# Kernel optimization log

Hardware: AMD Instinct MI355X
Metric: run time of the kernel (lower is better)

Reference implementation:

```python
import jax, jax.numpy as jnp
import numpy as np

NUM_HEADS = 16
EPS = 1e-6


def setup_inputs() -> dict:
    key = jax.random.key(0)
    ks = jax.random.split(key, 5)
    L, N, E = 2048, 8, 1024
    scale = 1.0 / np.sqrt(E)
    return {
        "query": jax.random.normal(ks[0], (L, N, E), jnp.float32),
        "Wq": jax.random.normal(ks[1], (E, E), jnp.float32) * scale,
        "Wk": jax.random.normal(ks[2], (E, E), jnp.float32) * scale,
        "Wv": jax.random.normal(ks[3], (E, E), jnp.float32) * scale,
        "Wo": jax.random.normal(ks[4], (E, E), jnp.float32) * scale,
    }


def reference(query, Wq, Wk, Wv, Wo):
    # cosFormer non-causal linear attention (self.causal = False branch).
    L, N, E = query.shape
    h = NUM_HEADS
    d = E // h

    # projections (nn.Linear, no bias) + ReLU feature map on q, k
    q = jax.nn.relu(query @ Wq.T)
    k = jax.nn.relu(query @ Wk.T)  # key defaults to query
    v = query @ Wv.T               # value defaults to query

    # (L, N, E) -> (n = N*h, L, d)
    def split_heads(x):
        return x.reshape(L, N * h, d).transpose(1, 0, 2)

    q, k, v = split_heads(q), split_heads(k), split_heads(v)

    # cos/sin reweighting: index = pi/2 * arange(1..m) / m, m = L (src==tgt)
    idx = (jnp.pi / 2) * jnp.arange(1, L + 1, dtype=jnp.float32) / L
    sin = jnp.sin(idx)[None, :, None]  # (1, L, 1)
    cos = jnp.cos(idx)[None, :, None]
    q_ = jnp.concatenate([q * sin, q * cos], axis=-1)  # (n, L, 2d)
    k_ = jnp.concatenate([k * sin, k * cos], axis=-1)

    # linear attention aggregation: kv_ is only (n, 2d, d)
    kv = jnp.einsum('nld,nlm->ndm', k_, v)
    z = 1.0 / jnp.maximum(jnp.einsum('nld,nd->nl', q_, k_.sum(axis=1)), EPS)
    attn = jnp.einsum('nld,ndm->nlm', q_, kv) * z[..., None]  # (n, L, d)

    # (n, L, d) -> (L, N, E), then output projection
    attn = attn.transpose(1, 0, 2).reshape(L, N, E)
    return attn @ Wo.T
```

## Files before the change

### kernel.cpp

```cpp
#include <hip/hip_runtime.h>
#include <math.h>

#define L_DIM 2048
#define N_DIM 8
#define E_DIM 1024
#define H_DIM 16
#define D_DIM 64
#define M_DIM (L_DIM * N_DIM)
#define NHEADS (N_DIM * H_DIM)
#define TWO_D 128
#define K_DIM 1024
#define CH 4
#define LCH (L_DIM / CH)

#define KV_ELEMS (NHEADS * TWO_D * D_DIM)
#define KS_ELEMS (NHEADS * TWO_D)
#define CSTRIDE (KV_ELEMS + KS_ELEMS)

typedef __attribute__((ext_vector_type(8))) __bf16 bf16x8;
typedef __attribute__((ext_vector_type(4))) float f32x4;

__device__ __forceinline__ ushort f2bf(float x) {
    union { float f; unsigned u; } a; a.f = x;
    unsigned r = a.u + 0x7fffu + ((a.u >> 16) & 1u);
    return (ushort)(r >> 16);
}
__device__ __forceinline__ float bf2f(ushort h) {
    union { unsigned u; float f; } a; a.u = ((unsigned)h) << 16;
    return a.f;
}

__device__ __forceinline__ void gload_lds16(const void* g, void* l) {
    __builtin_amdgcn_global_load_lds((const __attribute__((address_space(1))) void*)g,
                                     (__attribute__((address_space(3))) void*)l, 16, 0, 0);
}

__global__ __launch_bounds__(256) void split_fp32(const float* __restrict__ in,
                                                  ushort* __restrict__ hi,
                                                  ushort* __restrict__ lo, int n4) {
    int i = blockIdx.x * 256 + threadIdx.x;
    const int stride = gridDim.x * 256;
    for (; i < n4; i += stride) {
        float4 v = ((const float4*)in)[i];
        ushort h0 = f2bf(v.x), h1 = f2bf(v.y), h2 = f2bf(v.z), h3 = f2bf(v.w);
        ushort l0 = f2bf(v.x - bf2f(h0)), l1 = f2bf(v.y - bf2f(h1));
        ushort l2 = f2bf(v.z - bf2f(h2)), l3 = f2bf(v.w - bf2f(h3));
        ((ushort4*)hi)[i] = make_ushort4(h0, h1, h2, h3);
        ((ushort4*)lo)[i] = make_ushort4(l0, l1, l2, l3);
    }
}

__global__ __launch_bounds__(256) void split_w4(const float* __restrict__ w0,
                                                const float* __restrict__ w1,
                                                const float* __restrict__ w2,
                                                const float* __restrict__ w3,
                                                ushort* __restrict__ hi,
                                                ushort* __restrict__ lo) {
    const int midx = blockIdx.y;
    const float* src = (midx == 0) ? w0 : (midx == 1) ? w1 : (midx == 2) ? w2 : w3;
    hi += (size_t)midx * E_DIM * E_DIM;
    lo += (size_t)midx * E_DIM * E_DIM;
    const int n4 = E_DIM * E_DIM / 4;
    int i = blockIdx.x * 256 + threadIdx.x;
    const int stride = gridDim.x * 256;
    for (; i < n4; i += stride) {
        float4 v = ((const float4*)src)[i];
        ushort h0 = f2bf(v.x), h1 = f2bf(v.y), h2 = f2bf(v.z), h3 = f2bf(v.w);
        ushort l0 = f2bf(v.x - bf2f(h0)), l1 = f2bf(v.y - bf2f(h1));
        ushort l2 = f2bf(v.z - bf2f(h2)), l3 = f2bf(v.w - bf2f(h3));
        ((ushort4*)hi)[i] = make_ushort4(h0, h1, h2, h3);
        ((ushort4*)lo)[i] = make_ushort4(l0, l1, l2, l3);
    }
}

template <int OUTMODE, int NBS>
__global__ __launch_bounds__(512, 2) void gemm2(const ushort* __restrict__ Ahi,
                                                const ushort* __restrict__ Alo,
                                                const ushort* __restrict__ Bhi,
                                                const ushort* __restrict__ Blo,
                                                float* __restrict__ C,
                                                float* __restrict__ C2) {
    __shared__ ushort smem[2][32768];

    const int t = threadIdx.x;
    const int wid = t >> 6;
    const int lane = t & 63;

    const int x = blockIdx.x;
    const int cxcd = x & 7;
    const int j = x >> 3;
    const int mb = cxcd * 8 + j / NBS;
    const int nb = j % NBS;
    const int m0 = mb * 256, n0 = nb * 256;

    const int srow = t >> 2;
    const int sch = t & 3;
    const int gch = sch ^ ((srow >> 1) & 3);
    const size_t aOff = (size_t)(m0 + srow) * K_DIM + gch * 8;
    const size_t bOff = (size_t)(n0 + srow) * K_DIM + gch * 8;
    const size_t H128 = (size_t)128 * K_DIM;

#define STAGE(b, kt1)                                             \
    do {                                                          \
        const size_t kc_ = (size_t)(kt1) * 32;                    \
        ushort* d = (ushort*)&smem[b][0] + wid * 512;             \
        gload_lds16(Ahi + aOff + kc_, d);                         \
        gload_lds16(Ahi + aOff + H128 + kc_, d + 4096);           \
        gload_lds16(Alo + aOff + kc_, d + 8192);                  \
        gload_lds16(Alo + aOff + H128 + kc_, d + 12288);          \
        gload_lds16(Bhi + bOff + kc_, d + 16384);                 \
        gload_lds16(Bhi + bOff + H128 + kc_, d + 20480);          \
        gload_lds16(Blo + bOff + kc_, d + 24576);                 \
        gload_lds16(Blo + bOff + H128 + kc_, d + 28672);          \
    } while (0)

    const int wm = wid >> 2;
    const int wn = wid & 3;
    const int lr = lane & 15;
    const int kc = lane >> 4;
    int aoff[8], boff[4];
#pragma unroll
    for (int m = 0; m < 8; ++m) {
        const int r = wm * 128 + m * 16 + lr;
        aoff[m] = r * 32 + ((kc ^ ((r >> 1) & 3)) << 3);
    }
#pragma unroll
    for (int n = 0; n < 4; ++n) {
        const int r = wn * 64 + n * 16 + lr;
        boff[n] = r * 32 + ((kc ^ ((r >> 1) & 3)) << 3);
    }

    f32x4 acc[8][4];
    const f32x4 zv = {0.f, 0.f, 0.f, 0.f};
#pragma unroll
    for (int m = 0; m < 8; ++m)
#pragma unroll
        for (int n = 0; n < 4; ++n) acc[m][n] = zv;

    const int NK = K_DIM / 32;

    STAGE(0, 0);
    __syncthreads();

#pragma unroll 1
    for (int kt = 0; kt < NK; ++kt) {
        const int cb = kt & 1;
        if (kt + 1 < NK) STAGE(cb ^ 1, kt + 1);

        const ushort* bb = smem[cb];
        bf16x8 bh[4], bl[4];
#pragma unroll
        for (int n = 0; n < 4; ++n) {
            bh[n] = *(const bf16x8*)&bb[16384 + boff[n]];
            bl[n] = *(const bf16x8*)&bb[24576 + boff[n]];
        }
#pragma unroll
        for (int m = 0; m < 8; ++m) {
            const bf16x8 ah = *(const bf16x8*)&bb[aoff[m]];
            const bf16x8 al = *(const bf16x8*)&bb[8192 + aoff[m]];
#pragma unroll
            for (int n = 0; n < 4; ++n) {
                acc[m][n] = __builtin_amdgcn_mfma_f32_16x16x32_bf16(ah, bh[n], acc[m][n], 0, 0, 0);
                acc[m][n] = __builtin_amdgcn_mfma_f32_16x16x32_bf16(ah, bl[n], acc[m][n], 0, 0, 0);
                acc[m][n] = __builtin_amdgcn_mfma_f32_16x16x32_bf16(al, bh[n], acc[m][n], 0, 0, 0);
            }
        }
        __syncthreads();
    }

    const int erow = (lane >> 4) * 4;
    const int ecol = lane & 15;
#pragma unroll
    for (int m = 0; m < 8; ++m) {
        const int grb = m0 + wm * 128 + m * 16 + erow;
#pragma unroll
        for (int n = 0; n < 4; ++n) {
            const int gc = n0 + wn * 64 + n * 16 + ecol;
            f32x4 v = acc[m][n];
#pragma unroll
            for (int q = 0; q < 4; ++q) {
                const int gr = grb + q;
                float val = v[q];
                if constexpr (OUTMODE == 0) {
                    C[(size_t)gr * E_DIM + gc] = val;
                } else if constexpr (OUTMODE == 1) {
                    val = fmaxf(val, 0.f);
                    const int hh = gc >> 6, d = gc & 63;
                    C[((size_t)((gr & 7) * 16 + hh) * L_DIM + (gr >> 3)) * D_DIM + d] = val;
                } else {
                    const int mat = gc >> 10;
                    const int col = gc & 1023;
                    if (mat == 0) val = fmaxf(val, 0.f);
                    const int hh = col >> 6, d = col & 63;
                    float* dstc = mat ? C2 : C;
                    dstc[((size_t)((gr & 7) * 16 + hh) * L_DIM + (gr >> 3)) * D_DIM + d] = val;
                }
            }
        }
    }
#undef STAGE
}

__global__ __launch_bounds__(256) void kv_partial(const float* __restrict__ Kh,
                                                  const float* __restrict__ Vh,
                                                  float* __restrict__ kvp) {
    const int g = blockIdx.x;
    const int c = blockIdx.y;
    const int t = threadIdx.x;

    __shared__ float Kt[32][64];
    __shared__ float Vt[32][64];
    __shared__ float sT[32], cT[32];

    const int gi = t >> 3;
    const int gj = t & 7;
    const int i0 = gi * 2, j0 = gj * 8;

    float S[2][8], Cc[2][8];
#pragma unroll
    for (int i = 0; i < 2; ++i)
#pragma unroll
        for (int jj = 0; jj < 8; ++jj) { S[i][jj] = 0.f; Cc[i][jj] = 0.f; }
    float sk[2] = {0.f, 0.f}, ck[2] = {0.f, 0.f};

    for (int lt = 0; lt < LCH; lt += 32) {
        const int lbase = c * LCH + lt;
        const float4* ks = (const float4*)&Kh[((size_t)g * L_DIM + lbase) * D_DIM];
        const float4* vs = (const float4*)&Vh[((size_t)g * L_DIM + lbase) * D_DIM];
        ((float4*)&Kt[0][0])[t] = ks[t];
        ((float4*)&Kt[0][0])[t + 256] = ks[t + 256];
        ((float4*)&Vt[0][0])[t] = vs[t];
        ((float4*)&Vt[0][0])[t + 256] = vs[t + 256];
        if (t < 32) {
            const float ang = 1.57079632679489662f * (float)(lbase + t + 1) / (float)L_DIM;
            sT[t] = sinf(ang);
            cT[t] = cosf(ang);
        }
        __syncthreads();
#pragma unroll 4
        for (int lr = 0; lr < 32; ++lr) {
            const float sl = sT[lr], cl = cT[lr];
            const float k0v = Kt[lr][i0], k1v = Kt[lr][i0 + 1];
            const float ks0 = k0v * sl, ks1 = k1v * sl;
            const float kc0 = k0v * cl, kc1 = k1v * cl;
            sk[0] += ks0; sk[1] += ks1; ck[0] += kc0; ck[1] += kc1;
            float v8[8];
            *(float4*)&v8[0] = *(float4*)&Vt[lr][j0];
            *(float4*)&v8[4] = *(float4*)&Vt[lr][j0 + 4];
#pragma unroll
            for (int jj = 0; jj < 8; ++jj) {
                S[0][jj] = fmaf(ks0, v8[jj], S[0][jj]);
                S[1][jj] = fmaf(ks1, v8[jj], S[1][jj]);
                Cc[0][jj] = fmaf(kc0, v8[jj], Cc[0][jj]);
                Cc[1][jj] = fmaf(kc1, v8[jj], Cc[1][jj]);
            }
        }
        __syncthreads();
    }

    float* kvb = kvp + (size_t)c * CSTRIDE + (size_t)g * TWO_D * D_DIM;
#pragma unroll
    for (int ii = 0; ii < 2; ++ii) {
        *(float4*)&kvb[(size_t)(i0 + ii) * D_DIM + j0] =
            make_float4(S[ii][0], S[ii][1], S[ii][2], S[ii][3]);
        *(float4*)&kvb[(size_t)(i0 + ii) * D_DIM + j0 + 4] =
            make_float4(S[ii][4], S[ii][5], S[ii][6], S[ii][7]);
        *(float4*)&kvb[(size_t)(64 + i0 + ii) * D_DIM + j0] =
            make_float4(Cc[ii][0], Cc[ii][1], Cc[ii][2], Cc[ii][3]);
        *(float4*)&kvb[(size_t)(64 + i0 + ii) * D_DIM + j0 + 4] =
            make_float4(Cc[ii][4], Cc[ii][5], Cc[ii][6], Cc[ii][7]);
    }
    if (gj == 0) {
        float* ksb = kvp + (size_t)c * CSTRIDE + KV_ELEMS + (size_t)g * TWO_D;
        ksb[i0] = sk[0];
        ksb[i0 + 1] = sk[1];
        ksb[64 + i0] = ck[0];
        ksb[64 + i0 + 1] = ck[1];
    }
}

__global__ __launch_bounds__(256) void attn_kernel(const float* __restrict__ Qh,
                                                   const float* __restrict__ kvp,
                                                   ushort* __restrict__ attnHi,
                                                   ushort* __restrict__ attnLo) {
    const int g = blockIdx.x;
    const int lt = blockIdx.y;
    const int nb = g >> 4, hh = g & 15;
    const int t = threadIdx.x;

    __shared__ float kvs[TWO_D][64];
    __shared__ float qT[TWO_D][64];
    __shared__ float sTab[64], cTab[64], ksS[TWO_D], pz[64][4], zs[64];

    {
        const float4* kv4 = (const float4*)(kvp + (size_t)g * TWO_D * D_DIM);
        const size_t cs4 = CSTRIDE / 4;
        float4* kvs4 = (float4*)&kvs[0][0];
        for (int s = t; s < TWO_D * D_DIM / 4; s += 256) {
            float4 a = kv4[s], b = kv4[s + cs4], c = kv4[s + 2 * cs4], d = kv4[s + 3 * cs4];
            kvs4[s] = make_float4(a.x + b.x + c.x + d.x, a.y + b.y + c.y + d.y,
                                  a.z + b.z + c.z + d.z, a.w + b.w + c.w + d.w);
        }
    }
    if (t < TWO_D) {
        const size_t o = KV_ELEMS + (size_t)g * TWO_D + t;
        ksS[t] = kvp[o] + kvp[o + CSTRIDE] + kvp[o + 2 * (size_t)CSTRIDE] + kvp[o + 3 * (size_t)CSTRIDE];
    }

    const int lbase = lt * 64;
    if (t < 64) {
        const float ang = 1.57079632679489662f * (float)(lbase + t + 1) / (float)L_DIM;
        sTab[t] = sinf(ang);
        cTab[t] = cosf(ang);
    }

    const int lq = t >> 2;
    const int dq = (t & 3) * 16;
    float qv[16];
    {
        const float* qrow = Qh + ((size_t)g * L_DIM + lbase + lq) * D_DIM + dq;
        *(float4*)&qv[0] = *(const float4*)&qrow[0];
        *(float4*)&qv[4] = *(const float4*)&qrow[4];
        *(float4*)&qv[8] = *(const float4*)&qrow[8];
        *(float4*)&qv[12] = *(const float4*)&qrow[12];
    }
    __syncthreads();

    {
        const float sl = sTab[lq], cl = cTab[lq];
#pragma unroll
        for (int jj = 0; jj < 16; ++jj) {
            qT[dq + jj][lq] = qv[jj] * sl;
            qT[64 + dq + jj][lq] = qv[jj] * cl;
        }
    }
    __syncthreads();

    {
        const int lz = t >> 2, qz = t & 3;
        float p = 0.f;
#pragma unroll
        for (int i = 0; i < 32; ++i) p = fmaf(qT[qz * 32 + i][lz], ksS[qz * 32 + i], p);
        pz[lz][qz] = p;
    }
    __syncthreads();
    if (t < 64) {
        const float s = pz[t][0] + pz[t][1] + pz[t][2] + pz[t][3];
        zs[t] = 1.0f / fmaxf(s, 1e-6f);
    }
    __syncthreads();

    const int ml = (t >> 4) * 4;
    const int nd = (t & 15) * 4;
    float acc[4][4];
#pragma unroll
    for (int i = 0; i < 4; ++i)
#pragma unroll
        for (int jj = 0; jj < 4; ++jj) acc[i][jj] = 0.f;

    for (int i = 0; i < TWO_D; ++i) {
        float4 a = *(float4*)&qT[i][ml];
        float4 b = *(float4*)&kvs[i][nd];
        acc[0][0] = fmaf(a.x, b.x, acc[0][0]); acc[0][1] = fmaf(a.x, b.y, acc[0][1]);
        acc[0][2] = fmaf(a.x, b.z, acc[0][2]); acc[0][3] = fmaf(a.x, b.w, acc[0][3]);
        acc[1][0] = fmaf(a.y, b.x, acc[1][0]); acc[1][1] = fmaf(a.y, b.y, acc[1][1]);
        acc[1][2] = fmaf(a.y, b.z, acc[1][2]); acc[1][3] = fmaf(a.y, b.w, acc[1][3]);
        acc[2][0] = fmaf(a.z, b.x, acc[2][0]); acc[2][1] = fmaf(a.z, b.y, acc[2][1]);
        acc[2][2] = fmaf(a.z, b.z, acc[2][2]); acc[2][3] = fmaf(a.z, b.w, acc[2][3]);
        acc[3][0] = fmaf(a.w, b.x, acc[3][0]); acc[3][1] = fmaf(a.w, b.y, acc[3][1]);
        acc[3][2] = fmaf(a.w, b.z, acc[3][2]); acc[3][3] = fmaf(a.w, b.w, acc[3][3]);
    }

#pragma unroll
    for (int r = 0; r < 4; ++r) {
        const float z = zs[ml + r];
        const float o0 = acc[r][0] * z, o1 = acc[r][1] * z;
        const float o2 = acc[r][2] * z, o3 = acc[r][3] * z;
        ushort4 hv, lv;
        hv.x = f2bf(o0); lv.x = f2bf(o0 - bf2f(hv.x));
        hv.y = f2bf(o1); lv.y = f2bf(o1 - bf2f(hv.y));
        hv.z = f2bf(o2); lv.z = f2bf(o2 - bf2f(hv.z));
        hv.w = f2bf(o3); lv.w = f2bf(o3 - bf2f(hv.w));
        const size_t base = (size_t)((lbase + ml + r) * N_DIM + nb) * E_DIM + hh * 64 + nd;
        *(ushort4*)&attnHi[base] = hv;
        *(ushort4*)&attnLo[base] = lv;
    }
}

extern "C" void kernel_launch(void* const* d_in, const int* in_sizes, int n_in,
                              void* d_out, int out_size, void* d_ws, size_t ws_size,
                              hipStream_t stream) {
    const float* X = (const float*)d_in[0];
    const float* Wq = (const float*)d_in[1];
    const float* Wk = (const float*)d_in[2];
    const float* Wv = (const float*)d_in[3];
    const float* Wo = (const float*)d_in[4];
    float* out = (float*)d_out;

    char* ws = (char*)d_ws;
    ushort* Xhi = (ushort*)(ws + 0);
    ushort* Xlo = (ushort*)(ws + 33554432);
    ushort* Whi = (ushort*)(ws + 67108864);
    ushort* Wlo = (ushort*)(ws + 75497472);
    float* kvp  = (float*)(ws + 83886080);
    float* bufA = (float*)(ws + 100925440);

    float* Kh = out;
    float* Vh = bufA;
    float* Qh = out;

    const size_t WMAT = (size_t)E_DIM * E_DIM;

    split_fp32<<<2048, 256, 0, stream>>>(X, Xhi, Xlo, M_DIM * E_DIM / 4);
    split_w4<<<dim3(64, 4), 256, 0, stream>>>(Wq, Wk, Wv, Wo, Whi, Wlo);

    gemm2<2, 8><<<512, 512, 0, stream>>>(Xhi, Xlo, Whi + 1 * WMAT, Wlo + 1 * WMAT, Kh, Vh);

    kv_partial<<<dim3(NHEADS, CH), 256, 0, stream>>>(Kh, Vh, kvp);

    gemm2<1, 4><<<256, 512, 0, stream>>>(Xhi, Xlo, Whi + 0 * WMAT, Wlo + 0 * WMAT, Qh, nullptr);

    attn_kernel<<<dim3(NHEADS, L_DIM / 64), 256, 0, stream>>>(Qh, kvp, Xhi, Xlo);

    gemm2<0, 4><<<256, 512, 0, stream>>>(Xhi, Xlo, Whi + 3 * WMAT, Wlo + 3 * WMAT, out, nullptr);
}
```

Baseline: 538.0 us.

## Load GEMM B fragments straight from global into registers, halving LDS

The B operand (weights hi/lo) is no longer staged through shared memory. Each wave loads its B fragments directly from global memory into registers, double-buffered across two register sets, and the k-loop is unrolled by two. This halves LDS use per block and removes the B LDS reads. In exchange it adds register pressure and uncoalesced global reads of B, since the 4 waves sharing a wn column each fetch the same B data separately.

```diff
diff --git a/kernel.cpp b/kernel.cpp
--- a/kernel.cpp
+++ b/kernel.cpp
@@ -73,6 +73,35 @@
     }
 }
 
+__device__ __forceinline__ void loadB(const ushort* __restrict__ bH,
+                                      const ushort* __restrict__ bL,
+                                      int kt, bf16x8 bh[4], bf16x8 bl[4]) {
+    const size_t o = (size_t)kt * 32;
+    const size_t RS = (size_t)16 * K_DIM;
+#pragma unroll
+    for (int n = 0; n < 4; ++n) {
+        bh[n] = *(const bf16x8*)(bH + (size_t)n * RS + o);
+        bl[n] = *(const bf16x8*)(bL + (size_t)n * RS + o);
+    }
+}
+
+__device__ __forceinline__ void computeA(const ushort* __restrict__ bb,
+                                         const int* aoff,
+                                         const bf16x8 bh[4], const bf16x8 bl[4],
+                                         f32x4 acc[8][4]) {
+#pragma unroll
+    for (int m = 0; m < 8; ++m) {
+        const bf16x8 ah = *(const bf16x8*)&bb[aoff[m]];
+        const bf16x8 al = *(const bf16x8*)&bb[8192 + aoff[m]];
+#pragma unroll
+        for (int n = 0; n < 4; ++n) {
+            acc[m][n] = __builtin_amdgcn_mfma_f32_16x16x32_bf16(ah, bh[n], acc[m][n], 0, 0, 0);
+            acc[m][n] = __builtin_amdgcn_mfma_f32_16x16x32_bf16(ah, bl[n], acc[m][n], 0, 0, 0);
+            acc[m][n] = __builtin_amdgcn_mfma_f32_16x16x32_bf16(al, bh[n], acc[m][n], 0, 0, 0);
+        }
+    }
+}
+
 template <int OUTMODE, int NBS>
 __global__ __launch_bounds__(512, 2) void gemm2(const ushort* __restrict__ Ahi,
                                                 const ushort* __restrict__ Alo,
@@ -80,7 +109,7 @@
                                                 const ushort* __restrict__ Blo,
                                                 float* __restrict__ C,
                                                 float* __restrict__ C2) {
-    __shared__ ushort smem[2][32768];
+    __shared__ ushort smem[2][16384];
 
     const int t = threadIdx.x;
     const int wid = t >> 6;
@@ -97,10 +126,9 @@
     const int sch = t & 3;
     const int gch = sch ^ ((srow >> 1) & 3);
     const size_t aOff = (size_t)(m0 + srow) * K_DIM + gch * 8;
-    const size_t bOff = (size_t)(n0 + srow) * K_DIM + gch * 8;
     const size_t H128 = (size_t)128 * K_DIM;
 
-#define STAGE(b, kt1)                                             \
+#define STAGE_A(b, kt1)                                           \
     do {                                                          \
         const size_t kc_ = (size_t)(kt1) * 32;                    \
         ushort* d = (ushort*)&smem[b][0] + wid * 512;             \
@@ -108,27 +136,22 @@
         gload_lds16(Ahi + aOff + H128 + kc_, d + 4096);           \
         gload_lds16(Alo + aOff + kc_, d + 8192);                  \
         gload_lds16(Alo + aOff + H128 + kc_, d + 12288);          \
-        gload_lds16(Bhi + bOff + kc_, d + 16384);                 \
-        gload_lds16(Bhi + bOff + H128 + kc_, d + 20480);          \
-        gload_lds16(Blo + bOff + kc_, d + 24576);                 \
-        gload_lds16(Blo + bOff + H128 + kc_, d + 28672);          \
     } while (0)
 
     const int wm = wid >> 2;
     const int wn = wid & 3;
     const int lr = lane & 15;
     const int kc = lane >> 4;
-    int aoff[8], boff[4];
+    int aoff[8];
 #pragma unroll
     for (int m = 0; m < 8; ++m) {
         const int r = wm * 128 + m * 16 + lr;
         aoff[m] = r * 32 + ((kc ^ ((r >> 1) & 3)) << 3);
     }
-#pragma unroll
-    for (int n = 0; n < 4; ++n) {
-        const int r = wn * 64 + n * 16 + lr;
-        boff[n] = r * 32 + ((kc ^ ((r >> 1) & 3)) << 3);
-    }
+
+    const int brow = n0 + wn * 64 + lr;
+    const ushort* bH = Bhi + (size_t)brow * K_DIM + kc * 8;
+    const ushort* bL = Blo + (size_t)brow * K_DIM + kc * 8;
 
     f32x4 acc[8][4];
     const f32x4 zv = {0.f, 0.f, 0.f, 0.f};
@@ -139,32 +162,23 @@
 
     const int NK = K_DIM / 32;
 
-    STAGE(0, 0);
+    bf16x8 bhA[4], blA[4], bhB[4], blB[4];
+    STAGE_A(0, 0);
+    loadB(bH, bL, 0, bhA, blA);
     __syncthreads();
 
 #pragma unroll 1
-    for (int kt = 0; kt < NK; ++kt) {
-        const int cb = kt & 1;
-        if (kt + 1 < NK) STAGE(cb ^ 1, kt + 1);
-
-        const ushort* bb = smem[cb];
-        bf16x8 bh[4], bl[4];
-#pragma unroll
-        for (int n = 0; n < 4; ++n) {
-            bh[n] = *(const bf16x8*)&bb[16384 + boff[n]];
-            bl[n] = *(const bf16x8*)&bb[24576 + boff[n]];
-        }
-#pragma unroll
-        for (int m = 0; m < 8; ++m) {
-            const bf16x8 ah = *(const bf16x8*)&bb[aoff[m]];
-            const bf16x8 al = *(const bf16x8*)&bb[8192 + aoff[m]];
-#pragma unroll
-            for (int n = 0; n < 4; ++n) {
-                acc[m][n] = __builtin_amdgcn_mfma_f32_16x16x32_bf16(ah, bh[n], acc[m][n], 0, 0, 0);
-                acc[m][n] = __builtin_amdgcn_mfma_f32_16x16x32_bf16(ah, bl[n], acc[m][n], 0, 0, 0);
-                acc[m][n] = __builtin_amdgcn_mfma_f32_16x16x32_bf16(al, bh[n], acc[m][n], 0, 0, 0);
-            }
-        }
+    for (int kt = 0; kt < NK; kt += 2) {
+        STAGE_A(1, kt + 1);
+        loadB(bH, bL, kt + 1, bhB, blB);
+        computeA(&smem[0][0], aoff, bhA, blA, acc);
+        __syncthreads();
+
+        if (kt + 2 < NK) {
+            STAGE_A(0, kt + 2);
+            loadB(bH, bL, kt + 2, bhA, blA);
+        }
+        computeA(&smem[1][0], aoff, bhB, blB, acc);
         __syncthreads();
     }
 
@@ -198,7 +212,7 @@
             }
         }
     }
-#undef STAGE
+#undef STAGE_A
 }
 
 __global__ __launch_bounds__(256) void kv_partial(const float* __restrict__ Kh,
```

New measurement: 677.0 us. 1.26x slower.

## Use split-bf16 MFMA for attention output and amortize kv load across tiles

Applied to the files above, without the earlier changes.

The scalar FP32 q·kv product in the attention kernel is replaced by bf16 MFMA 16x16x32 using a hi/lo split with three products to keep near-FP32 accuracy. Each block now handles four 64-row L tiles, so the reduced kv matrix is summed and converted once per four tiles, using swizzled LDS layouts to avoid bank conflicts. The normalizer dot product is computed directly in registers without the transposed qT buffer. The risks are fewer blocks in flight (a quarter of the grid), scalar 2-byte output stores, and small precision loss from the dropped lo×lo term.

```diff
diff --git a/kernel.cpp b/kernel.cpp
--- a/kernel.cpp
+++ b/kernel.cpp
@@ -19,6 +19,7 @@
 
 typedef __attribute__((ext_vector_type(8))) __bf16 bf16x8;
 typedef __attribute__((ext_vector_type(4))) float f32x4;
+typedef __attribute__((ext_vector_type(8))) ushort u16x8;
 
 __device__ __forceinline__ ushort f2bf(float x) {
     union { float f; unsigned u; } a; a.f = x;
@@ -279,111 +280,153 @@
     }
 }
 
-__global__ __launch_bounds__(256) void attn_kernel(const float* __restrict__ Qh,
-                                                   const float* __restrict__ kvp,
-                                                   ushort* __restrict__ attnHi,
-                                                   ushort* __restrict__ attnLo) {
+__global__ __launch_bounds__(256) void attn_mfma(const float* __restrict__ Qh,
+                                                 const float* __restrict__ kvp,
+                                                 ushort* __restrict__ attnHi,
+                                                 ushort* __restrict__ attnLo) {
     const int g = blockIdx.x;
-    const int lt = blockIdx.y;
+    const int ltg = blockIdx.y;
     const int nb = g >> 4, hh = g & 15;
     const int t = threadIdx.x;
-
-    __shared__ float kvs[TWO_D][64];
-    __shared__ float qT[TWO_D][64];
-    __shared__ float sTab[64], cTab[64], ksS[TWO_D], pz[64][4], zs[64];
-
-    {
-        const float4* kv4 = (const float4*)(kvp + (size_t)g * TWO_D * D_DIM);
-        const size_t cs4 = CSTRIDE / 4;
-        float4* kvs4 = (float4*)&kvs[0][0];
-        for (int s = t; s < TWO_D * D_DIM / 4; s += 256) {
-            float4 a = kv4[s], b = kv4[s + cs4], c = kv4[s + 2 * cs4], d = kv4[s + 3 * cs4];
-            kvs4[s] = make_float4(a.x + b.x + c.x + d.x, a.y + b.y + c.y + d.y,
-                                  a.z + b.z + c.z + d.z, a.w + b.w + c.w + d.w);
-        }
-    }
+    const int wid = t >> 6, lane = t & 63;
+
+    __shared__ ushort kvbH[4][64][32];
+    __shared__ ushort kvbL[4][64][32];
+    __shared__ ushort qaH[4][64][32];
+    __shared__ ushort qaL[4][64][32];
+    __shared__ float ksS[TWO_D];
+    __shared__ float pz[64][4];
+    __shared__ float zs[64];
+
     if (t < TWO_D) {
         const size_t o = KV_ELEMS + (size_t)g * TWO_D + t;
-        ksS[t] = kvp[o] + kvp[o + CSTRIDE] + kvp[o + 2 * (size_t)CSTRIDE] + kvp[o + 3 * (size_t)CSTRIDE];
-    }
-
-    const int lbase = lt * 64;
-    if (t < 64) {
-        const float ang = 1.57079632679489662f * (float)(lbase + t + 1) / (float)L_DIM;
-        sTab[t] = sinf(ang);
-        cTab[t] = cosf(ang);
+        ksS[t] = kvp[o] + kvp[o + CSTRIDE] + kvp[o + 2 * (size_t)CSTRIDE] +
+                 kvp[o + 3 * (size_t)CSTRIDE];
+    }
+
+    {
+        const float* kvg = kvp + (size_t)g * TWO_D * D_DIM;
+        const int d = t & 63;
+        const int igb = t >> 6;
+        const int csd = (d >> 1) & 3;
+#pragma unroll
+        for (int rep = 0; rep < 4; ++rep) {
+            const int i0 = (rep * 4 + igb) * 8;
+            float v[8];
+#pragma unroll
+            for (int jj = 0; jj < 8; ++jj) {
+                const size_t o = (size_t)(i0 + jj) * D_DIM + d;
+                v[jj] = kvg[o] + kvg[o + CSTRIDE] + kvg[o + 2 * (size_t)CSTRIDE] +
+                        kvg[o + 3 * (size_t)CSTRIDE];
+            }
+            const int ks = i0 >> 5;
+            const int cs = ((((i0 >> 3) & 3) ^ csd) << 3);
+            u16x8 h, l;
+#pragma unroll
+            for (int jj = 0; jj < 8; ++jj) {
+                h[jj] = f2bf(v[jj]);
+                l[jj] = f2bf(v[jj] - bf2f(h[jj]));
+            }
+            *(u16x8*)&kvbH[ks][d][cs] = h;
+            *(u16x8*)&kvbL[ks][d][cs] = l;
+        }
     }
 
     const int lq = t >> 2;
     const int dq = (t & 3) * 16;
-    float qv[16];
-    {
+    const int csq = (lq >> 1) & 3;
+
+    const int lr = lane & 15, kc = lane >> 4;
+    const int arow = wid * 16 + lr;
+    const int aco = ((kc ^ ((arow >> 1) & 3)) << 3);
+    int bro[4], bco[4];
+#pragma unroll
+    for (int n = 0; n < 4; ++n) {
+        bro[n] = n * 16 + lr;
+        bco[n] = ((kc ^ ((bro[n] >> 1) & 3)) << 3);
+    }
+    const int erow = (lane >> 4) * 4;
+    const int ecol = lane & 15;
+
+    __syncthreads();
+
+#pragma unroll 1
+    for (int it = 0; it < 4; ++it) {
+        const int lbase = (ltg * 4 + it) * 64;
+
+        float qv[16];
         const float* qrow = Qh + ((size_t)g * L_DIM + lbase + lq) * D_DIM + dq;
         *(float4*)&qv[0] = *(const float4*)&qrow[0];
         *(float4*)&qv[4] = *(const float4*)&qrow[4];
         *(float4*)&qv[8] = *(const float4*)&qrow[8];
         *(float4*)&qv[12] = *(const float4*)&qrow[12];
-    }
-    __syncthreads();
-
-    {
-        const float sl = sTab[lq], cl = cTab[lq];
-#pragma unroll
-        for (int jj = 0; jj < 16; ++jj) {
-            qT[dq + jj][lq] = qv[jj] * sl;
-            qT[64 + dq + jj][lq] = qv[jj] * cl;
-        }
-    }
-    __syncthreads();
-
-    {
-        const int lz = t >> 2, qz = t & 3;
+        const float ang = 1.57079632679489662f * (float)(lbase + lq + 1) / (float)L_DIM;
+        const float sl = sinf(ang), cl = cosf(ang);
+
         float p = 0.f;
 #pragma unroll
-        for (int i = 0; i < 32; ++i) p = fmaf(qT[qz * 32 + i][lz], ksS[qz * 32 + i], p);
-        pz[lz][qz] = p;
-    }
-    __syncthreads();
-    if (t < 64) {
-        const float s = pz[t][0] + pz[t][1] + pz[t][2] + pz[t][3];
-        zs[t] = 1.0f / fmaxf(s, 1e-6f);
-    }
-    __syncthreads();
-
-    const int ml = (t >> 4) * 4;
-    const int nd = (t & 15) * 4;
-    float acc[4][4];
-#pragma unroll
-    for (int i = 0; i < 4; ++i)
-#pragma unroll
-        for (int jj = 0; jj < 4; ++jj) acc[i][jj] = 0.f;
-
-    for (int i = 0; i < TWO_D; ++i) {
-        float4 a = *(float4*)&qT[i][ml];
-        float4 b = *(float4*)&kvs[i][nd];
-        acc[0][0] = fmaf(a.x, b.x, acc[0][0]); acc[0][1] = fmaf(a.x, b.y, acc[0][1]);
-        acc[0][2] = fmaf(a.x, b.z, acc[0][2]); acc[0][3] = fmaf(a.x, b.w, acc[0][3]);
-        acc[1][0] = fmaf(a.y, b.x, acc[1][0]); acc[1][1] = fmaf(a.y, b.y, acc[1][1]);
-        acc[1][2] = fmaf(a.y, b.z, acc[1][2]); acc[1][3] = fmaf(a.y, b.w, acc[1][3]);
-        acc[2][0] = fmaf(a.z, b.x, acc[2][0]); acc[2][1] = fmaf(a.z, b.y, acc[2][1]);
-        acc[2][2] = fmaf(a.z, b.z, acc[2][2]); acc[2][3] = fmaf(a.z, b.w, acc[2][3]);
-        acc[3][0] = fmaf(a.w, b.x, acc[3][0]); acc[3][1] = fmaf(a.w, b.y, acc[3][1]);
-        acc[3][2] = fmaf(a.w, b.z, acc[3][2]); acc[3][3] = fmaf(a.w, b.w, acc[3][3]);
-    }
-
-#pragma unroll
-    for (int r = 0; r < 4; ++r) {
-        const float z = zs[ml + r];
-        const float o0 = acc[r][0] * z, o1 = acc[r][1] * z;
-        const float o2 = acc[r][2] * z, o3 = acc[r][3] * z;
-        ushort4 hv, lv;
-        hv.x = f2bf(o0); lv.x = f2bf(o0 - bf2f(hv.x));
-        hv.y = f2bf(o1); lv.y = f2bf(o1 - bf2f(hv.y));
-        hv.z = f2bf(o2); lv.z = f2bf(o2 - bf2f(hv.z));
-        hv.w = f2bf(o3); lv.w = f2bf(o3 - bf2f(hv.w));
-        const size_t base = (size_t)((lbase + ml + r) * N_DIM + nb) * E_DIM + hh * 64 + nd;
-        *(ushort4*)&attnHi[base] = hv;
-        *(ushort4*)&attnLo[base] = lv;
+        for (int jj = 0; jj < 16; ++jj)
+            p += qv[jj] * (sl * ksS[dq + jj] + cl * ksS[64 + dq + jj]);
+        pz[lq][t & 3] = p;
+
+#pragma unroll
+        for (int jg = 0; jg < 2; ++jg) {
+            const int ib = dq + jg * 8;
+            const int ks = ib >> 5;
+            const int cs = ((((ib >> 3) & 3) ^ csq) << 3);
+            u16x8 hs, ls, hc, lc;
+#pragma unroll
+            for (int jj = 0; jj < 8; ++jj) {
+                const float vs = qv[jg * 8 + jj] * sl;
+                const float vc = qv[jg * 8 + jj] * cl;
+                hs[jj] = f2bf(vs); ls[jj] = f2bf(vs - bf2f(hs[jj]));
+                hc[jj] = f2bf(vc); lc[jj] = f2bf(vc - bf2f(hc[jj]));
+            }
+            *(u16x8*)&qaH[ks][lq][cs] = hs;
+            *(u16x8*)&qaL[ks][lq][cs] = ls;
+            *(u16x8*)&qaH[ks + 2][lq][cs] = hc;
+            *(u16x8*)&qaL[ks + 2][lq][cs] = lc;
+        }
+        __syncthreads();
+        if (t < 64) {
+            const float s = pz[t][0] + pz[t][1] + pz[t][2] + pz[t][3];
+            zs[t] = 1.0f / fmaxf(s, 1e-6f);
+        }
+        __syncthreads();
+
+        f32x4 acc[4];
+        const f32x4 zv = {0.f, 0.f, 0.f, 0.f};
+#pragma unroll
+        for (int n = 0; n < 4; ++n) acc[n] = zv;
+#pragma unroll
+        for (int ks = 0; ks < 4; ++ks) {
+            const bf16x8 ah = *(const bf16x8*)&qaH[ks][arow][aco];
+            const bf16x8 al = *(const bf16x8*)&qaL[ks][arow][aco];
+#pragma unroll
+            for (int n = 0; n < 4; ++n) {
+                const bf16x8 bh = *(const bf16x8*)&kvbH[ks][bro[n]][bco[n]];
+                const bf16x8 bl = *(const bf16x8*)&kvbL[ks][bro[n]][bco[n]];
+                acc[n] = __builtin_amdgcn_mfma_f32_16x16x32_bf16(ah, bh, acc[n], 0, 0, 0);
+                acc[n] = __builtin_amdgcn_mfma_f32_16x16x32_bf16(ah, bl, acc[n], 0, 0, 0);
+                acc[n] = __builtin_amdgcn_mfma_f32_16x16x32_bf16(al, bh, acc[n], 0, 0, 0);
+            }
+        }
+
+#pragma unroll
+        for (int n = 0; n < 4; ++n) {
+#pragma unroll
+            for (int q = 0; q < 4; ++q) {
+                const int lrow = wid * 16 + erow + q;
+                const float val = acc[n][q] * zs[lrow];
+                const int d = n * 16 + ecol;
+                const ushort hv = f2bf(val);
+                const ushort lv = f2bf(val - bf2f(hv));
+                const size_t base = (size_t)((lbase + lrow) * N_DIM + nb) * E_DIM + hh * 64 + d;
+                attnHi[base] = hv;
+                attnLo[base] = lv;
+            }
+        }
+        __syncthreads();
     }
 }
 
@@ -420,7 +463,7 @@
 
     gemm2<1, 4><<<256, 512, 0, stream>>>(Xhi, Xlo, Whi + 0 * WMAT, Wlo + 0 * WMAT, Qh, nullptr);
 
-    attn_kernel<<<dim3(NHEADS, L_DIM / 64), 256, 0, stream>>>(Qh, kvp, Xhi, Xlo);
+    attn_mfma<<<dim3(NHEADS, L_DIM / 256), 256, 0, stream>>>(Qh, kvp, Xhi, Xlo);
 
     gemm2<0, 4><<<256, 512, 0, stream>>>(Xhi, Xlo, Whi + 3 * WMAT, Wlo + 3 * WMAT, out, nullptr);
 }
```

Measured after the change: 467.5 us. 1.15x faster.
